# Optimization experiments

Measured on AMD Instinct MI355X. Metric: run time of the kernel, lower is better.

## Reference

```python
import jax, jax.numpy as jnp
import numpy as np

EPS_COMBINE = float(np.finfo(float).eps)  # combined[combined == 0] = np.finfo(float).eps
LOSS_COEF = 0.01


def cv_squared(v):
    # torch .var() is unbiased -> ddof=1
    return jnp.var(v, ddof=1) / (jnp.mean(v) ** 2 + 1e-10)


def setup_inputs() -> dict:
    key = jax.random.key(0)
    k1, k2, k3, k4 = jax.random.split(key, 4)
    B, D, E, C = 4096, 1024, 8, 4096
    x = jax.random.normal(k1, (B, D), jnp.float32)
    # small scale so exp(expert_out) in combine() stays finite
    w_gate = jax.random.normal(k2, (D, E), jnp.float32) * 0.02
    w_exp = jax.random.normal(k3, (E, D, C), jnp.float32) * 0.02
    b_exp = jax.random.normal(k4, (E, C), jnp.float32) * 0.02
    return {"x": x, "w_gate": w_gate, "w_exp": w_exp, "b_exp": b_exp, "k": 4}


def reference(x, w_gate, w_exp, b_exp, k):
    B, D = x.shape
    E = w_gate.shape[1]
    # --- noisy_top_k_gating with noisy_gating=False ---
    logits = x @ w_gate                                   # [B, E]
    top_logits, top_idx = jax.lax.top_k(logits, min(k + 1, E))
    topk_logits = top_logits[:, :k]
    topk_idx = top_idx[:, :k]
    topk_gates = jax.nn.softmax(topk_logits, axis=1)      # softmax over top-k only
    gates = jnp.zeros((B, E), x.dtype).at[jnp.arange(B)[:, None], topk_idx].set(topk_gates)
    importance = gates.sum(0)
    load = (gates > 0).sum(0).astype(jnp.float32)         # _gates_to_load
    loss = (cv_squared(importance) + cv_squared(load)) * LOSS_COEF
    # --- dispatch + per-expert forward + weighted combine ---
    # Experts with gate==0 contribute exactly 0 to the combine, so the dense
    # einsum over all experts computes the same math as SparseDispatcher.
    expert_out = jnp.einsum('bd,edc->bec', x, w_exp) + b_exp   # [B, E, C]
    combined = jnp.einsum('bec,be->bc', jnp.exp(expert_out), gates)  # weighted scatter-combine
    combined = jnp.where(combined == 0, EPS_COMBINE, combined)
    y = jnp.log(combined)
    return y, loss
```

## Files before the change

kernel.cpp:

```cpp
#include <hip/hip_runtime.h>
#include <stdint.h>

#define B_ROWS 4096
#define D_DIM  1024
#define E_NUM  8
#define C_DIM  4096
#define LOSS_COEF 0.01f
#define EPS_COMBINE 2.220446049250313e-16f

typedef float  f32x4  __attribute__((ext_vector_type(4)));
typedef __bf16 bf16x8 __attribute__((ext_vector_type(8)));

static __device__ __forceinline__ unsigned short f2bf(float f) {
    unsigned int u = __float_as_uint(f);
    u += 0x7fffu + ((u >> 16) & 1u);
    return (unsigned short)(u >> 16);
}

static __device__ __forceinline__ void async16(const void* g, void* l) {
    __builtin_amdgcn_global_load_lds(
        (const __attribute__((address_space(1))) unsigned int*)g,
        (__attribute__((address_space(3))) unsigned int*)l, 16, 0, 0);
}

#define TP_BLOCKS (8 * 8 * 32)

__global__ __launch_bounds__(256) void prep_kernel(
    const float* __restrict__ x,
    const float* __restrict__ wg,
    const float* __restrict__ wexp,
    unsigned short* __restrict__ xb,
    unsigned short* __restrict__ wT,
    float* __restrict__ gates,
    float* __restrict__ stats)
{
    const int t = threadIdx.x;
    if ((int)blockIdx.x < TP_BLOCKS) {
        __shared__ unsigned short Tt[128 * 128];
        const int bid = blockIdx.x;
        const int ct = bid & 31;
        const int kt = (bid >> 5) & 7;
        const int e  = bid >> 8;
        const int k0 = kt * 128, c0 = ct * 128;
        const float* src = wexp + ((size_t)e * D_DIM + k0) * C_DIM + c0;

        #pragma unroll
        for (int i = 0; i < 16; ++i) {
            const int kr = i * 8 + (t >> 5);
            const int g  = t & 31;
            float4 v = *(const float4*)(src + (size_t)kr * C_DIM + g * 4);
            unsigned short h[4] = { f2bf(v.x), f2bf(v.y), f2bf(v.z), f2bf(v.w) };
            const int gp = g ^ (((kr >> 4) & 7) << 1);
            *(uint2*)&Tt[kr * 128 + gp * 4] = *(const uint2*)h;
        }
        __syncthreads();

        unsigned short* dst = wT + (size_t)e * C_DIM * D_DIM
                            + (size_t)c0 * D_DIM + k0;
        #pragma unroll
        for (int i = 0; i < 4; ++i) {
            const int task = i * 256 + t;
            const int kch  = task & 7;
            const int c    = task >> 3;
            const int g    = c >> 2;
            unsigned short hh[16];
            #pragma unroll
            for (int j = 0; j < 16; ++j) {
                const int k  = kch * 16 + j;
                const int gp = g ^ (((k >> 4) & 7) << 1);
                hh[j] = Tt[k * 128 + gp * 4 + (c & 3)];
            }
            *(uint4*)(dst + (size_t)c * D_DIM + kch * 16)     = ((const uint4*)hh)[0];
            *(uint4*)(dst + (size_t)c * D_DIM + kch * 16 + 8) = ((const uint4*)hh)[1];
        }
    } else {
        __shared__ float simp[E_NUM], sload[E_NUM];
        if (t < E_NUM) { simp[t] = 0.0f; sload[t] = 0.0f; }
        __syncthreads();
        const int lane = t & 63;
        const int wid  = t >> 6;
        const int row  = ((int)blockIdx.x - TP_BLOCKS) * 4 + wid;

        float acc[8] = {0.f,0.f,0.f,0.f,0.f,0.f,0.f,0.f};
        #pragma unroll
        for (int i = 0; i < 4; ++i) {
            int d = i * 256 + lane * 4;
            float4 xv = *(const float4*)(x + (size_t)row * D_DIM + d);
            unsigned short hh[4] = { f2bf(xv.x), f2bf(xv.y), f2bf(xv.z), f2bf(xv.w) };
            *(uint2*)(xb + (size_t)row * D_DIM + d) = *(const uint2*)hh;
            float xa[4] = { xv.x, xv.y, xv.z, xv.w };
            #pragma unroll
            for (int j = 0; j < 4; ++j) {
                const float4* wp = (const float4*)(wg + (size_t)(d + j) * 8);
                float4 w0 = wp[0], w1 = wp[1];
                acc[0] += xa[j] * w0.x; acc[1] += xa[j] * w0.y;
                acc[2] += xa[j] * w0.z; acc[3] += xa[j] * w0.w;
                acc[4] += xa[j] * w1.x; acc[5] += xa[j] * w1.y;
                acc[6] += xa[j] * w1.z; acc[7] += xa[j] * w1.w;
            }
        }
        #pragma unroll
        for (int off = 32; off > 0; off >>= 1)
            #pragma unroll
            for (int e = 0; e < 8; ++e)
                acc[e] += __shfl_xor(acc[e], off, 64);
        if (lane == 0) {
            float val[4]; int idx[4]; unsigned used = 0;
            #pragma unroll
            for (int j = 0; j < 4; ++j) {
                float best = -1e30f; int bi = 0;
                for (int ee = 0; ee < 8; ++ee)
                    if (!(used & (1u << ee)) && acc[ee] > best) { best = acc[ee]; bi = ee; }
                used |= 1u << bi; val[j] = best; idx[j] = bi;
            }
            float mx = val[0], sum = 0.f, gv[4];
            #pragma unroll
            for (int j = 0; j < 4; ++j) { gv[j] = __expf(val[j] - mx); sum += gv[j]; }
            float inv = 1.0f / sum;
            float gout[8] = {0.f,0.f,0.f,0.f,0.f,0.f,0.f,0.f};
            #pragma unroll
            for (int j = 0; j < 4; ++j) gout[idx[j]] = gv[j] * inv;
            #pragma unroll
            for (int e = 0; e < 8; ++e) gates[(size_t)row * 8 + e] = gout[e];
            #pragma unroll
            for (int j = 0; j < 4; ++j) {
                atomicAdd(&simp[idx[j]], gv[j] * inv);
                atomicAdd(&sload[idx[j]], 1.0f);
            }
        }
        __syncthreads();
        if (t < E_NUM) {
            atomicAdd(&stats[t],          simp[t]);
            atomicAdd(&stats[E_NUM + t],  sload[t]);
        }
    }
}

__global__ void loss_kernel(const float* __restrict__ stats, float* __restrict__ out_loss) {
    if (threadIdx.x == 0) {
        float mi = 0.f, ml = 0.f;
        for (int e = 0; e < 8; ++e) { mi += stats[e]; ml += stats[8 + e]; }
        mi *= 0.125f; ml *= 0.125f;
        float vi = 0.f, vl = 0.f;
        for (int e = 0; e < 8; ++e) {
            float a = stats[e] - mi;     vi += a * a;
            float b = stats[8 + e] - ml; vl += b * b;
        }
        vi *= (1.0f / 7.0f); vl *= (1.0f / 7.0f);
        out_loss[0] = (vi / (mi * mi + 1e-10f) + vl / (ml * ml + 1e-10f)) * LOSS_COEF;
    }
}

__global__ __launch_bounds__(256, 3) void moe_main_kernel(
    const unsigned short* __restrict__ xb,
    const unsigned short* __restrict__ wT,
    const float* __restrict__ bexp,
    const float* __restrict__ gates,
    float* __restrict__ out)
{
    __shared__ unsigned short As[128 * 32];
    __shared__ unsigned short Bs[2 * 64 * 32];
    __shared__ float gs[128 * 9];
    __shared__ float bs[8 * 64];

    const int tid  = threadIdx.x;
    const int lane = tid & 63;
    const int wid  = tid >> 6;
    const int wm   = wid >> 1;
    const int wn   = wid & 1;
    const int q    = lane >> 4;
    const int ln   = lane & 15;
    const int row0 = blockIdx.x * 128;
    const int col0 = blockIdx.y * 64;

    #pragma unroll
    for (int i = 0; i < 4; ++i) {
        int idx = i * 256 + tid;
        gs[(idx >> 3) * 9 + (idx & 7)] = gates[(size_t)row0 * 8 + idx];
    }
    {
        int e = tid >> 5, c = tid & 31;
        bs[e * 64 + c]      = bexp[(size_t)e * C_DIM + col0 + c];
        bs[e * 64 + c + 32] = bexp[(size_t)e * C_DIM + col0 + c + 32];
    }

    const int rS = tid >> 2;
    const int qg = (tid & 3) ^ (rS & 3);
    const unsigned short* gA  = xb + (size_t)(row0 + rS) * D_DIM + qg * 8;
    const unsigned short* gBb = wT + (size_t)(col0 + rS) * D_DIM + qg * 8;
    char* ldsA = (char*)As + wid * 1024;
    char* ldsB = (char*)Bs + wid * 1024;

    const int fq = ((q ^ (ln & 3)) << 3);

    const f32x4 vzero = {0.f, 0.f, 0.f, 0.f};
    f32x4 comb[4][2];
    #pragma unroll
    for (int i = 0; i < 4; ++i)
        #pragma unroll
        for (int j = 0; j < 2; ++j) comb[i][j] = vzero;

    for (int eg = 0; eg < 4; ++eg) {
        f32x4 acc[4][2][2];
        #pragma unroll
        for (int i = 0; i < 4; ++i)
            #pragma unroll
            for (int j = 0; j < 2; ++j)
                #pragma unroll
                for (int e = 0; e < 2; ++e) acc[i][j][e] = vzero;

        const unsigned short* gB0 = gBb + (size_t)(2 * eg)     * C_DIM * D_DIM;
        const unsigned short* gB1 = gBb + (size_t)(2 * eg + 1) * C_DIM * D_DIM;

        for (int kt = 0; kt < D_DIM / 32; ++kt) {
            const int ko = kt * 32;
            async16(gA + ko,               ldsA);
            async16(gA + ko + 64 * D_DIM,  ldsA + 4096);
            async16(gB0 + ko,              ldsB);
            async16(gB1 + ko,              ldsB + 4096);

            __syncthreads();

            bf16x8 af[4], bfr[2][2];
            #pragma unroll
            for (int fm = 0; fm < 4; ++fm)
                af[fm] = *(const bf16x8*)(As + (wm * 64 + fm * 16 + ln) * 32 + fq);
            #pragma unroll
            for (int fn = 0; fn < 2; ++fn)
                #pragma unroll
                for (int e = 0; e < 2; ++e)
                    bfr[fn][e] = *(const bf16x8*)(Bs + e * 2048 +
                                    (wn * 32 + fn * 16 + ln) * 32 + fq);
            #pragma unroll
            for (int fm = 0; fm < 4; ++fm)
                #pragma unroll
                for (int fn = 0; fn < 2; ++fn)
                    #pragma unroll
                    for (int e = 0; e < 2; ++e)
                        acc[fm][fn][e] = __builtin_amdgcn_mfma_f32_16x16x32_bf16(
                            af[fm], bfr[fn][e], acc[fm][fn][e], 0, 0, 0);

            __syncthreads();
        }

        #pragma unroll
        for (int e = 0; e < 2; ++e) {
            int eG = eg * 2 + e;
            #pragma unroll
            for (int fn = 0; fn < 2; ++fn) {
                float bval = bs[eG * 64 + wn * 32 + fn * 16 + ln];
                #pragma unroll
                for (int fm = 0; fm < 4; ++fm)
                    #pragma unroll
                    for (int r = 0; r < 4; ++r) {
                        float g = gs[(wm * 64 + fm * 16 + q * 4 + r) * 9 + eG];
                        comb[fm][fn][r] += g * __expf(acc[fm][fn][e][r] + bval);
                    }
            }
        }
    }

    #pragma unroll
    for (int fm = 0; fm < 4; ++fm)
        #pragma unroll
        for (int fn = 0; fn < 2; ++fn)
            #pragma unroll
            for (int r = 0; r < 4; ++r) {
                int row = row0 + wm * 64 + fm * 16 + q * 4 + r;
                int col = col0 + wn * 32 + fn * 16 + ln;
                float c = comb[fm][fn][r];
                c = (c == 0.0f) ? EPS_COMBINE : c;
                out[(size_t)row * C_DIM + col] = __logf(c);
            }
}

extern "C" void kernel_launch(void* const* d_in, const int* in_sizes, int n_in,
                              void* d_out, int out_size, void* d_ws, size_t ws_size,
                              hipStream_t stream) {
    const float* x    = (const float*)d_in[0];
    const float* wg   = (const float*)d_in[1];
    const float* wexp = (const float*)d_in[2];
    const float* bexp = (const float*)d_in[3];
    float* out = (float*)d_out;
    char*  ws  = (char*)d_ws;

    unsigned short* wT    = (unsigned short*)ws;
    unsigned short* xb    = (unsigned short*)(ws + 67108864);
    float*          gates = (float*)(ws + 75497472);
    float*          stats = (float*)(ws + 75628544);

    hipMemsetAsync(stats, 0, 16 * sizeof(float), stream);
    prep_kernel<<<TP_BLOCKS + B_ROWS / 4, 256, 0, stream>>>(
        x, wg, wexp, xb, wT, gates, stats);
    loss_kernel<<<1, 64, 0, stream>>>(stats, out + (size_t)B_ROWS * C_DIM);

    dim3 grid(B_ROWS / 128, C_DIM / 64);
    moe_main_kernel<<<grid, 256, 0, stream>>>(xb, wT, bexp, gates, out);
}
```

Before: 558.8 us.

## Retile weight transpose tiles and compute loss stats from gates in a separate reduction

The weight transpose/convert tile changes from 128x128 to 256(k)x64(c) with a new swizzle, so each thread writes one 16-byte chunk and stores along k are longer and contiguous. The shared and global atomics for importance/load, the memset, and the stats buffer are removed. The loss kernel now reduces the gates array itself with wave shuffles and runs after the main kernel. This trims a memset launch and atomic contention, at the cost of a 256-thread block rereading 128KB of gates.

```diff
diff --git a/kernel.cpp b/kernel.cpp
--- a/kernel.cpp
+++ b/kernel.cpp
@@ -23,7 +23,7 @@
         (__attribute__((address_space(3))) unsigned int*)l, 16, 0, 0);
 }
 
-#define TP_BLOCKS (8 * 8 * 32)
+#define TP_BLOCKS 2048
 
 __global__ __launch_bounds__(256) void prep_kernel(
     const float* __restrict__ x,
@@ -31,52 +31,43 @@
     const float* __restrict__ wexp,
     unsigned short* __restrict__ xb,
     unsigned short* __restrict__ wT,
-    float* __restrict__ gates,
-    float* __restrict__ stats)
+    float* __restrict__ gates)
 {
     const int t = threadIdx.x;
     if ((int)blockIdx.x < TP_BLOCKS) {
-        __shared__ unsigned short Tt[128 * 128];
+        __shared__ unsigned short Tt[256 * 64];
         const int bid = blockIdx.x;
-        const int ct = bid & 31;
-        const int kt = (bid >> 5) & 7;
+        const int ct = bid & 63;
+        const int kt = (bid >> 6) & 3;
         const int e  = bid >> 8;
-        const int k0 = kt * 128, c0 = ct * 128;
+        const int k0 = kt * 256, c0 = ct * 64;
         const float* src = wexp + ((size_t)e * D_DIM + k0) * C_DIM + c0;
 
         #pragma unroll
         for (int i = 0; i < 16; ++i) {
-            const int kr = i * 8 + (t >> 5);
-            const int g  = t & 31;
-            float4 v = *(const float4*)(src + (size_t)kr * C_DIM + g * 4);
+            const int kr = i * 16 + (t >> 4);
+            const int cg = (t & 15) * 4;
+            float4 v = *(const float4*)(src + (size_t)kr * C_DIM + cg);
             unsigned short h[4] = { f2bf(v.x), f2bf(v.y), f2bf(v.z), f2bf(v.w) };
-            const int gp = g ^ (((kr >> 4) & 7) << 1);
-            *(uint2*)&Tt[kr * 128 + gp * 4] = *(const uint2*)h;
+            const int cswz = cg ^ (((kr >> 3) & 15) << 2);
+            *(uint2*)&Tt[kr * 64 + cswz] = *(const uint2*)h;
         }
         __syncthreads();
 
-        unsigned short* dst = wT + (size_t)e * C_DIM * D_DIM
-                            + (size_t)c0 * D_DIM + k0;
-        #pragma unroll
-        for (int i = 0; i < 4; ++i) {
+        unsigned short* dstb = wT + (size_t)e * C_DIM * D_DIM + k0;
+        #pragma unroll
+        for (int i = 0; i < 8; ++i) {
             const int task = i * 256 + t;
-            const int kch  = task & 7;
-            const int c    = task >> 3;
-            const int g    = c >> 2;
-            unsigned short hh[16];
-            #pragma unroll
-            for (int j = 0; j < 16; ++j) {
-                const int k  = kch * 16 + j;
-                const int gp = g ^ (((k >> 4) & 7) << 1);
-                hh[j] = Tt[k * 128 + gp * 4 + (c & 3)];
-            }
-            *(uint4*)(dst + (size_t)c * D_DIM + kch * 16)     = ((const uint4*)hh)[0];
-            *(uint4*)(dst + (size_t)c * D_DIM + kch * 16 + 8) = ((const uint4*)hh)[1];
+            const int ko8  = task & 31;
+            const int c    = task >> 5;
+            const int cswz = c ^ ((ko8 & 15) << 2);
+            unsigned short hh[8];
+            #pragma unroll
+            for (int j = 0; j < 8; ++j)
+                hh[j] = Tt[(ko8 * 8 + j) * 64 + cswz];
+            *(uint4*)(dstb + (size_t)(c0 + c) * D_DIM + ko8 * 8) = *(const uint4*)hh;
         }
     } else {
-        __shared__ float simp[E_NUM], sload[E_NUM];
-        if (t < E_NUM) { simp[t] = 0.0f; sload[t] = 0.0f; }
-        __syncthreads();
         const int lane = t & 63;
         const int wid  = t >> 6;
         const int row  = ((int)blockIdx.x - TP_BLOCKS) * 4 + wid;
@@ -122,29 +113,49 @@
             for (int j = 0; j < 4; ++j) gout[idx[j]] = gv[j] * inv;
             #pragma unroll
             for (int e = 0; e < 8; ++e) gates[(size_t)row * 8 + e] = gout[e];
-            #pragma unroll
-            for (int j = 0; j < 4; ++j) {
-                atomicAdd(&simp[idx[j]], gv[j] * inv);
-                atomicAdd(&sload[idx[j]], 1.0f);
-            }
-        }
-        __syncthreads();
-        if (t < E_NUM) {
-            atomicAdd(&stats[t],          simp[t]);
-            atomicAdd(&stats[E_NUM + t],  sload[t]);
-        }
-    }
-}
-
-__global__ void loss_kernel(const float* __restrict__ stats, float* __restrict__ out_loss) {
-    if (threadIdx.x == 0) {
+        }
+    }
+}
+
+__global__ __launch_bounds__(256) void loss_kernel(
+    const float* __restrict__ gates, float* __restrict__ out_loss) {
+    __shared__ float sI[4][8], sC[4][8];
+    const int t = threadIdx.x, lane = t & 63, wid = t >> 6;
+    float imp[8] = {0,0,0,0,0,0,0,0}, cnt[8] = {0,0,0,0,0,0,0,0};
+    for (int r = t; r < B_ROWS; r += 256) {
+        const float4* gp = (const float4*)(gates + (size_t)r * 8);
+        float4 g0 = gp[0], g1 = gp[1];
+        imp[0] += g0.x; imp[1] += g0.y; imp[2] += g0.z; imp[3] += g0.w;
+        imp[4] += g1.x; imp[5] += g1.y; imp[6] += g1.z; imp[7] += g1.w;
+        cnt[0] += (g0.x > 0.f); cnt[1] += (g0.y > 0.f);
+        cnt[2] += (g0.z > 0.f); cnt[3] += (g0.w > 0.f);
+        cnt[4] += (g1.x > 0.f); cnt[5] += (g1.y > 0.f);
+        cnt[6] += (g1.z > 0.f); cnt[7] += (g1.w > 0.f);
+    }
+    #pragma unroll
+    for (int off = 32; off > 0; off >>= 1)
+        #pragma unroll
+        for (int e = 0; e < 8; ++e) {
+            imp[e] += __shfl_xor(imp[e], off, 64);
+            cnt[e] += __shfl_xor(cnt[e], off, 64);
+        }
+    if (lane == 0)
+        #pragma unroll
+        for (int e = 0; e < 8; ++e) { sI[wid][e] = imp[e]; sC[wid][e] = cnt[e]; }
+    __syncthreads();
+    if (t == 0) {
+        float I[8], C[8];
+        for (int e = 0; e < 8; ++e) {
+            I[e] = sI[0][e] + sI[1][e] + sI[2][e] + sI[3][e];
+            C[e] = sC[0][e] + sC[1][e] + sC[2][e] + sC[3][e];
+        }
         float mi = 0.f, ml = 0.f;
-        for (int e = 0; e < 8; ++e) { mi += stats[e]; ml += stats[8 + e]; }
+        for (int e = 0; e < 8; ++e) { mi += I[e]; ml += C[e]; }
         mi *= 0.125f; ml *= 0.125f;
         float vi = 0.f, vl = 0.f;
         for (int e = 0; e < 8; ++e) {
-            float a = stats[e] - mi;     vi += a * a;
-            float b = stats[8 + e] - ml; vl += b * b;
+            float a = I[e] - mi; vi += a * a;
+            float b = C[e] - ml; vl += b * b;
         }
         vi *= (1.0f / 7.0f); vl *= (1.0f / 7.0f);
         out_loss[0] = (vi / (mi * mi + 1e-10f) + vl / (ml * ml + 1e-10f)) * LOSS_COEF;
@@ -287,13 +298,12 @@
     unsigned short* wT    = (unsigned short*)ws;
     unsigned short* xb    = (unsigned short*)(ws + 67108864);
     float*          gates = (float*)(ws + 75497472);
-    float*          stats = (float*)(ws + 75628544);
-
-    hipMemsetAsync(stats, 0, 16 * sizeof(float), stream);
+
     prep_kernel<<<TP_BLOCKS + B_ROWS / 4, 256, 0, stream>>>(
-        x, wg, wexp, xb, wT, gates, stats);
-    loss_kernel<<<1, 64, 0, stream>>>(stats, out + (size_t)B_ROWS * C_DIM);
+        x, wg, wexp, xb, wT, gates);
 
     dim3 grid(B_ROWS / 128, C_DIM / 64);
     moe_main_kernel<<<grid, 256, 0, stream>>>(xb, wT, bexp, gates, out);
-}
+
+    loss_kernel<<<1, 256, 0, stream>>>(gates, out + (size_t)B_ROWS * C_DIM);
+}
```

Result: no change. 564.8 us (+1.1%).
